# Optimization experiments

Hardware: AMD Instinct MI355X
Metric: run time of the kernel (lower is better)

The kernel has to match this reference:

```python
import jax, jax.numpy as jnp
import numpy as np
from jax import lax

N, P, Z, L = 1000, 50000, 10, 5


def setup_inputs() -> dict:
    key = jax.random.key(0)
    ks = jax.random.split(key, 9)
    data = jax.random.normal(ks[0], (N, P), dtype=jnp.float32)
    mean_z = jax.random.normal(ks[1], (N, Z), dtype=jnp.float32)
    A = jax.random.normal(ks[2], (Z, Z), dtype=jnp.float32) * 0.1
    var_z = A @ A.T + 0.01 * jnp.eye(Z, dtype=jnp.float32)  # PSD
    mean_w = jax.random.normal(ks[3], (L, Z, P), dtype=jnp.float32) * 0.01
    var_w = jax.random.uniform(ks[4], (L, Z), dtype=jnp.float32) + 0.1   # positive
    alpha = jax.nn.softmax(jax.random.normal(ks[5], (L, Z, P), dtype=jnp.float32), axis=-1)
    tau_0 = jax.random.uniform(ks[6], (L, Z), dtype=jnp.float32) + 0.5   # positive prior precision
    pi = jax.nn.softmax(jax.random.normal(ks[7], (Z, P), dtype=jnp.float32), axis=-1)
    tau = jnp.array(1.0, dtype=jnp.float32)
    return dict(data=data, mean_z=mean_z, var_z=var_z, mean_w=mean_w,
                var_w=var_w, alpha=alpha, tau_0=tau_0, pi=pi, tau=tau)


def _log_bf(z, s2, s0):
    s0_inv = 1.0 / s0
    s2ps0inv = s2 + s0_inv
    return 0.5 * (jnp.log(s2) - jnp.log(s2ps0inv) + z ** 2 * (s0_inv / s2ps0inv))


def reference(data, mean_z, var_z, mean_w, var_w, alpha, tau_0, pi, tau):
    n_dim = data.shape[0]
    l_dim, z_dim, p_dim = mean_w.shape

    # FactorModel.moments
    mean_zz = mean_z.T @ mean_z + n_dim * var_z            # [z, z]
    # LoadingModel.moments (only mean_w moment is needed)
    W0 = jnp.sum(mean_w * alpha, axis=0)                    # [z, p]

    def factor_body(kdx, carry):
        W, mw, vw, al = carry
        not_k = jnp.where(jnp.arange(z_dim) != kdx, size=z_dim - 1)[0]  # [z-1]
        E_zpzk = mean_zz[kdx][not_k]                        # [z-1]
        E_zzk = mean_zz[kdx, kdx]                           # scalar
        Wk = W[kdx]                                         # [p]
        Wnk = W[not_k]                                      # [z-1, p]
        RtZk = mean_z[:, kdx] @ data - Wnk.T @ E_zpzk       # [p]

        def effect_body(ldx, ecarry):
            Wk, mw, vw, al = ecarry
            Wkl = Wk - mw[ldx, kdx] * al[ldx, kdx]          # [p] residualized
            E_RtZk = RtZk - E_zzk * Wkl                     # [p]
            u_var = jnp.reciprocal(tau * E_zzk + tau_0[ldx, kdx])  # scalar
            u_mean = tau * u_var * E_RtZk                   # [p]
            Z_s = E_RtZk / E_zzk * jnp.sqrt(E_zzk * tau)    # [p]
            s2_s = 1.0 / (E_zzk * tau)
            log_bf = _log_bf(Z_s, s2_s, tau_0[ldx, kdx])
            alpha_kl = jax.nn.softmax(jnp.log(pi[kdx]) + log_bf)   # [p]
            Wk_new = Wkl + u_mean * alpha_kl
            return (Wk_new,
                    mw.at[ldx, kdx].set(u_mean),
                    vw.at[ldx, kdx].set(u_var),
                    al.at[ldx, kdx].set(alpha_kl))

        Wk, mw, vw, al = lax.fori_loop(0, l_dim, effect_body, (Wk, mw, vw, al))
        return (W.at[kdx].set(Wk), mw, vw, al)

    W, mw, vw, al = lax.fori_loop(0, z_dim, factor_body, (W0, mean_w, var_w, alpha))
    return mw, vw, al
```

## Files before the change

### kernel.cpp

```cpp
#include <hip/hip_runtime.h>
#include <math.h>

#define N_DIM 1000
#define P_DIM 50000
#define Z_DIM 10
#define L_DIM 5
#define NT 256
#define NB 196
#define NSPLIT 4
#define NCHUNK 250
#define NEG_BIG (-3.0e38f)

constexpr size_t ZP      = (size_t)Z_DIM * P_DIM;
constexpr size_t OFF_ZTR = 0;
constexpr size_t OFF_W   = ZP;
constexpr size_t OFF_WK  = 2 * ZP;
constexpr size_t OFF_RTZ = 2 * ZP + P_DIM;
constexpr size_t OFF_LG  = 2 * ZP + 2 * P_DIM;
constexpr size_t OFF_ZZ  = 2 * ZP + 3 * P_DIM;
constexpr size_t OFF_PM0 = OFF_ZZ + 128;
constexpr size_t OFF_PS0 = OFF_PM0 + NB;
constexpr size_t OFF_PM1 = OFF_PS0 + NB;
constexpr size_t OFF_PS1 = OFF_PM1 + NB;

constexpr size_t OUT_MW = 0;
constexpr size_t OUT_VW = (size_t)L_DIM * Z_DIM * P_DIM;
constexpr size_t OUT_AL = OUT_VW + (size_t)L_DIM * Z_DIM;

__device__ inline void online_merge(float& m, float& e, float m2, float e2) {
    float M = fmaxf(m, m2);
    e = e * __expf(m - M) + e2 * __expf(m2 - M);
    m = M;
}

__device__ inline void block_merge(float& m, float& e, float* sm, float* se, float* bro) {
    int lane = threadIdx.x & 63;
    int wid  = threadIdx.x >> 6;
    #pragma unroll
    for (int off = 32; off > 0; off >>= 1) {
        float m2 = __shfl_xor(m, off);
        float e2 = __shfl_xor(e, off);
        online_merge(m, e, m2, e2);
    }
    if (lane == 0) { sm[wid] = m; se[wid] = e; }
    __syncthreads();
    if (threadIdx.x == 0) {
        float M = sm[0], E = se[0];
        #pragma unroll
        for (int w = 1; w < NT / 64; w++) online_merge(M, E, sm[w], se[w]);
        bro[0] = M; bro[1] = E;
    }
    __syncthreads();
    m = bro[0]; e = bro[1];
}

__global__ __launch_bounds__(256) void init_zz(const float* __restrict__ mean_z,
                                               const float* __restrict__ var_z,
                                               float* __restrict__ ws) {
    float* zz = ws + OFF_ZZ;
    int i = blockIdx.x / Z_DIM, j = blockIdx.x % Z_DIM;
    float s = 0.f;
    for (int n = threadIdx.x; n < N_DIM; n += 256)
        s += mean_z[n * Z_DIM + i] * mean_z[n * Z_DIM + j];
    #pragma unroll
    for (int off = 32; off > 0; off >>= 1) s += __shfl_xor(s, off);
    __shared__ float ls[4];
    if ((threadIdx.x & 63) == 0) ls[threadIdx.x >> 6] = s;
    __syncthreads();
    if (threadIdx.x == 0) {
        float t = ls[0] + ls[1] + ls[2] + ls[3];
        zz[blockIdx.x] = t + (float)N_DIM * var_z[blockIdx.x];
    }
}

__global__ __launch_bounds__(NT) void precompute_big(const float* __restrict__ data,
                                                     const float* __restrict__ mean_z,
                                                     const float* __restrict__ mw0,
                                                     const float* __restrict__ al0,
                                                     float* __restrict__ ws) {
    float* ZtR = ws + OFF_ZTR;
    float* W   = ws + OFF_W;
    __shared__ float mzs[NCHUNK * Z_DIM];
    int n0 = blockIdx.y * NCHUNK;
    for (int i = threadIdx.x; i < NCHUNK * Z_DIM; i += NT)
        mzs[i] = mean_z[n0 * Z_DIM + i];
    __syncthreads();
    int p = blockIdx.x * NT + threadIdx.x;
    if (p >= P_DIM) return;

    float acc[Z_DIM];
    #pragma unroll
    for (int z = 0; z < Z_DIM; z++) acc[z] = 0.f;
    for (int r = 0; r < NCHUNK; r++) {
        float d = data[(size_t)(n0 + r) * P_DIM + p];
        #pragma unroll
        for (int z = 0; z < Z_DIM; z++) acc[z] += mzs[r * Z_DIM + z] * d;
    }
    #pragma unroll
    for (int z = 0; z < Z_DIM; z++) atomicAdd(&ZtR[(size_t)z * P_DIM + p], acc[z]);

    if (blockIdx.y == 0) {
        #pragma unroll
        for (int z = 0; z < Z_DIM; z++) {
            float w = 0.f;
            #pragma unroll
            for (int l = 0; l < L_DIM; l++) {
                size_t io = ((size_t)l * Z_DIM + z) * P_DIM + p;
                w += mw0[io] * al0[io];
            }
            W[(size_t)z * P_DIM + p] = w;
        }
    }
}

__global__ __launch_bounds__(NT) void step_kernel(const float* __restrict__ mw0,
                                                  const float* __restrict__ al0,
                                                  const float* __restrict__ pi,
                                                  const float* __restrict__ tau0,
                                                  const float* __restrict__ taup,
                                                  float* __restrict__ ws,
                                                  float* __restrict__ out,
                                                  int k, int l, int pk, int pl,
                                                  int has_prev, int prev_last, int s) {
    float* ZtR = ws + OFF_ZTR;
    float* W   = ws + OFF_W;
    float* Wk  = ws + OFF_WK;
    float* RtZ = ws + OFF_RTZ;
    float* lg  = ws + OFF_LG;
    float* zz  = ws + OFF_ZZ;
    int wbuf = s & 1, rbuf = 1 - wbuf;
    float* pm_r = ws + (rbuf ? OFF_PM1 : OFF_PM0);
    float* ps_r = ws + (rbuf ? OFF_PS1 : OFF_PS0);
    float* pm_w = ws + (wbuf ? OFF_PM1 : OFF_PM0);
    float* ps_w = ws + (wbuf ? OFF_PS1 : OFF_PS0);

    float* out_mw = out + OUT_MW;
    float* out_vw = out + OUT_VW;
    float* out_al = out + OUT_AL;

    __shared__ float sm[NT / 64], se[NT / 64], bro[2];

    int tid = threadIdx.x;
    int p = blockIdx.x * NT + tid;
    bool valid = p < P_DIM;
    float tau = taup[0];

    float wk = 0.f;

    if (has_prev) {
        float m = NEG_BIG, e = 0.f;
        if (tid < NB) { m = pm_r[tid]; e = ps_r[tid]; }
        block_merge(m, e, sm, se, bro);
        float M = m, S = e;
        if (valid) {
            float a = __expf(lg[p] - M) / S;
            size_t po = ((size_t)pl * Z_DIM + pk) * P_DIM + p;
            out_al[po] = a;
            float um = out_mw[po];
            wk = Wk[p] + um * a;
            if (prev_last) W[(size_t)pk * P_DIM + p] = wk;
        }
    }

    float Ezz   = zz[k * Z_DIM + k];
    float t0v   = tau0[l * Z_DIM + k];
    float u_var = 1.f / (tau * Ezz + t0v);
    float s2    = 1.f / (Ezz * tau);
    float s0inv = 1.f / t0v;
    float cq    = 0.5f * (tau / Ezz) * (s0inv / (s2 + s0inv));

    float r = 0.f;
    if (valid) {
        if (l == 0) {
            r = ZtR[(size_t)k * P_DIM + p];
            #pragma unroll
            for (int j = 0; j < Z_DIM; j++) {
                if (j == k) continue;
                float wj = (has_prev && prev_last && j == pk) ? wk
                                                              : W[(size_t)j * P_DIM + p];
                r -= zz[k * Z_DIM + j] * wj;
            }
            RtZ[p] = r;
            wk = W[(size_t)k * P_DIM + p];
        } else {
            r = RtZ[p];
        }
    }

    float m = NEG_BIG, e = 0.f;
    if (valid) {
        size_t io = ((size_t)l * Z_DIM + k) * P_DIM + p;
        float wkl = wk - mw0[io] * al0[io];
        float E   = r - Ezz * wkl;
        float um  = tau * u_var * E;
        float lgt = __logf(pi[(size_t)k * P_DIM + p]) + cq * E * E;
        out_mw[io] = um;
        lg[p] = lgt;
        Wk[p] = wkl;
        m = lgt; e = 1.f;
    }
    block_merge(m, e, sm, se, bro);
    if (tid == 0) { pm_w[blockIdx.x] = m; ps_w[blockIdx.x] = e; }
    if (tid == 0 && blockIdx.x == 0) out_vw[l * Z_DIM + k] = u_var;
}

__global__ __launch_bounds__(NT) void final_kernel(float* __restrict__ ws,
                                                   float* __restrict__ out, int s_last) {
    float* lg = ws + OFF_LG;
    int rbuf = s_last & 1;
    float* pm_r = ws + (rbuf ? OFF_PM1 : OFF_PM0);
    float* ps_r = ws + (rbuf ? OFF_PS1 : OFF_PS0);
    float* out_al = out + OUT_AL;

    __shared__ float sm[NT / 64], se[NT / 64], bro[2];
    int tid = threadIdx.x;
    int p = blockIdx.x * NT + tid;

    float m = NEG_BIG, e = 0.f;
    if (tid < NB) { m = pm_r[tid]; e = ps_r[tid]; }
    block_merge(m, e, sm, se, bro);
    if (p < P_DIM) {
        float a = __expf(lg[p] - m) / e;
        out_al[((size_t)4 * Z_DIM + 9) * P_DIM + p] = a;
    }
}

extern "C" void kernel_launch(void* const* d_in, const int* in_sizes, int n_in,
                              void* d_out, int out_size, void* d_ws, size_t ws_size,
                              hipStream_t stream) {
    (void)in_sizes; (void)n_in; (void)out_size; (void)ws_size;
    const float* data   = (const float*)d_in[0];
    const float* mean_z = (const float*)d_in[1];
    const float* var_z  = (const float*)d_in[2];
    const float* mw0    = (const float*)d_in[3];
    const float* al0    = (const float*)d_in[5];
    const float* tau0   = (const float*)d_in[6];
    const float* pi     = (const float*)d_in[7];
    const float* taup   = (const float*)d_in[8];
    float* out = (float*)d_out;
    float* ws  = (float*)d_ws;

    hipMemsetAsync(ws, 0, ZP * sizeof(float), stream);
    init_zz<<<Z_DIM * Z_DIM, 256, 0, stream>>>(mean_z, var_z, ws);
    precompute_big<<<dim3(NB, NSPLIT), NT, 0, stream>>>(data, mean_z, mw0, al0, ws);

    for (int s = 0; s < Z_DIM * L_DIM; s++) {
        int k = s / L_DIM, l = s % L_DIM;
        int pk = (s > 0) ? (s - 1) / L_DIM : 0;
        int pl = (s > 0) ? (s - 1) % L_DIM : 0;
        int has_prev  = (s > 0) ? 1 : 0;
        int prev_last = (has_prev && pl == L_DIM - 1) ? 1 : 0;
        step_kernel<<<NB, NT, 0, stream>>>(mw0, al0, pi, tau0, taup, ws, out,
                                           k, l, pk, pl, has_prev, prev_last, s);
    }
    final_kernel<<<NB, NT, 0, stream>>>(ws, out, Z_DIM * L_DIM - 1);
}
```

Baseline: 573.6 us.

## Replace per-step kernel launches with single persistent kernel using spin-wait grid reduction

Replaces the 50 step launches and the final kernel with one persistent kernel of 49 blocks of 1024 threads. Each thread keeps its W row and ZtR values in registers across all steps. Blocks publish their softmax partials as packed 64-bit atomics in workspace and spin-wait on them, so no kernel boundary is needed between steps. This removes launch overhead and the global round-trips for W, Wk, RtZ and lg. The cost is a busy-wait that assumes all 49 blocks are co-resident, and a bounded spin (SPIN_MAX) that could silently read incomplete data.

```diff
diff --git a/kernel.cpp b/kernel.cpp
--- a/kernel.cpp
+++ b/kernel.cpp
@@ -5,23 +5,24 @@
 #define P_DIM 50000
 #define Z_DIM 10
 #define L_DIM 5
-#define NT 256
-#define NB 196
+#define NSTEP 50
+
+#define NTP 256
+#define NBP 196
 #define NSPLIT 4
 #define NCHUNK 250
+
+#define NT1 1024
+#define NBLK 49
 #define NEG_BIG (-3.0e38f)
-
-constexpr size_t ZP      = (size_t)Z_DIM * P_DIM;
-constexpr size_t OFF_ZTR = 0;
-constexpr size_t OFF_W   = ZP;
-constexpr size_t OFF_WK  = 2 * ZP;
-constexpr size_t OFF_RTZ = 2 * ZP + P_DIM;
-constexpr size_t OFF_LG  = 2 * ZP + 2 * P_DIM;
-constexpr size_t OFF_ZZ  = 2 * ZP + 3 * P_DIM;
-constexpr size_t OFF_PM0 = OFF_ZZ + 128;
-constexpr size_t OFF_PS0 = OFF_PM0 + NB;
-constexpr size_t OFF_PM1 = OFF_PS0 + NB;
-constexpr size_t OFF_PS1 = OFF_PM1 + NB;
+#define SPIN_MAX 32768
+
+constexpr size_t ZP       = (size_t)Z_DIM * P_DIM;
+constexpr size_t OFF_ZTR  = 0;
+constexpr size_t OFF_PART = ZP;
+constexpr size_t PART_F   = (size_t)NSTEP * 64 * 2;
+constexpr size_t OFF_ZZ   = ZP + PART_F;
+constexpr size_t WS_ZERO_BYTES = (ZP + PART_F) * sizeof(float);
 
 constexpr size_t OUT_MW = 0;
 constexpr size_t OUT_VW = (size_t)L_DIM * Z_DIM * P_DIM;
@@ -31,27 +32,6 @@
     float M = fmaxf(m, m2);
     e = e * __expf(m - M) + e2 * __expf(m2 - M);
     m = M;
-}
-
-__device__ inline void block_merge(float& m, float& e, float* sm, float* se, float* bro) {
-    int lane = threadIdx.x & 63;
-    int wid  = threadIdx.x >> 6;
-    #pragma unroll
-    for (int off = 32; off > 0; off >>= 1) {
-        float m2 = __shfl_xor(m, off);
-        float e2 = __shfl_xor(e, off);
-        online_merge(m, e, m2, e2);
-    }
-    if (lane == 0) { sm[wid] = m; se[wid] = e; }
-    __syncthreads();
-    if (threadIdx.x == 0) {
-        float M = sm[0], E = se[0];
-        #pragma unroll
-        for (int w = 1; w < NT / 64; w++) online_merge(M, E, sm[w], se[w]);
-        bro[0] = M; bro[1] = E;
-    }
-    __syncthreads();
-    m = bro[0]; e = bro[1];
 }
 
 __global__ __launch_bounds__(256) void init_zz(const float* __restrict__ mean_z,
@@ -73,19 +53,16 @@
     }
 }
 
-__global__ __launch_bounds__(NT) void precompute_big(const float* __restrict__ data,
-                                                     const float* __restrict__ mean_z,
-                                                     const float* __restrict__ mw0,
-                                                     const float* __restrict__ al0,
-                                                     float* __restrict__ ws) {
+__global__ __launch_bounds__(NTP) void precompute_big(const float* __restrict__ data,
+                                                      const float* __restrict__ mean_z,
+                                                      float* __restrict__ ws) {
     float* ZtR = ws + OFF_ZTR;
-    float* W   = ws + OFF_W;
     __shared__ float mzs[NCHUNK * Z_DIM];
     int n0 = blockIdx.y * NCHUNK;
-    for (int i = threadIdx.x; i < NCHUNK * Z_DIM; i += NT)
+    for (int i = threadIdx.x; i < NCHUNK * Z_DIM; i += NTP)
         mzs[i] = mean_z[n0 * Z_DIM + i];
     __syncthreads();
-    int p = blockIdx.x * NT + threadIdx.x;
+    int p = blockIdx.x * NTP + threadIdx.x;
     if (p >= P_DIM) return;
 
     float acc[Z_DIM];
@@ -94,134 +71,152 @@
     for (int r = 0; r < NCHUNK; r++) {
         float d = data[(size_t)(n0 + r) * P_DIM + p];
         #pragma unroll
-        for (int z = 0; z < Z_DIM; z++) acc[z] += mzs[r * Z_DIM + z] * d;
+        for (int z = 0; z < Z_DIM; z++) acc[z] = fmaf(mzs[r * Z_DIM + z], d, acc[z]);
     }
     #pragma unroll
     for (int z = 0; z < Z_DIM; z++) atomicAdd(&ZtR[(size_t)z * P_DIM + p], acc[z]);
-
-    if (blockIdx.y == 0) {
-        #pragma unroll
-        for (int z = 0; z < Z_DIM; z++) {
-            float w = 0.f;
-            #pragma unroll
-            for (int l = 0; l < L_DIM; l++) {
-                size_t io = ((size_t)l * Z_DIM + z) * P_DIM + p;
-                w += mw0[io] * al0[io];
-            }
-            W[(size_t)z * P_DIM + p] = w;
-        }
-    }
-}
-
-__global__ __launch_bounds__(NT) void step_kernel(const float* __restrict__ mw0,
+}
+
+__global__ __launch_bounds__(NT1) void steps_coop(const float* __restrict__ mw0,
                                                   const float* __restrict__ al0,
                                                   const float* __restrict__ pi,
                                                   const float* __restrict__ tau0,
                                                   const float* __restrict__ taup,
                                                   float* __restrict__ ws,
-                                                  float* __restrict__ out,
-                                                  int k, int l, int pk, int pl,
-                                                  int has_prev, int prev_last, int s) {
-    float* ZtR = ws + OFF_ZTR;
-    float* W   = ws + OFF_W;
-    float* Wk  = ws + OFF_WK;
-    float* RtZ = ws + OFF_RTZ;
-    float* lg  = ws + OFF_LG;
-    float* zz  = ws + OFF_ZZ;
-    int wbuf = s & 1, rbuf = 1 - wbuf;
-    float* pm_r = ws + (rbuf ? OFF_PM1 : OFF_PM0);
-    float* ps_r = ws + (rbuf ? OFF_PS1 : OFF_PS0);
-    float* pm_w = ws + (wbuf ? OFF_PM1 : OFF_PM0);
-    float* ps_w = ws + (wbuf ? OFF_PS1 : OFF_PS0);
-
+                                                  float* __restrict__ out) {
+    const float* ZtR = ws + OFF_ZTR;
+    const float* zz  = ws + OFF_ZZ;
+    unsigned long long* part = reinterpret_cast<unsigned long long*>(ws + OFF_PART);
     float* out_mw = out + OUT_MW;
     float* out_vw = out + OUT_VW;
     float* out_al = out + OUT_AL;
 
-    __shared__ float sm[NT / 64], se[NT / 64], bro[2];
-
-    int tid = threadIdx.x;
-    int p = blockIdx.x * NT + tid;
-    bool valid = p < P_DIM;
-    float tau = taup[0];
-
-    float wk = 0.f;
-
-    if (has_prev) {
+    __shared__ float sm[NT1 / 64], se[NT1 / 64], bro[2];
+
+    const int tid  = threadIdx.x;
+    const int bid  = blockIdx.x;
+    const int lane = tid & 63;
+    const int wid  = tid >> 6;
+    const int p    = bid * NT1 + tid;
+    const bool valid = p < P_DIM;
+    const float tau = taup[0];
+
+    float W[Z_DIM], Zt[Z_DIM];
+    #pragma unroll
+    for (int z = 0; z < Z_DIM; z++) { W[z] = 0.f; Zt[z] = 0.f; }
+    float mw_c = 0.f, al_c = 0.f, lpi = 0.f;
+    if (valid) {
+        #pragma unroll
+        for (int z = 0; z < Z_DIM; z++) Zt[z] = ZtR[(size_t)z * P_DIM + p];
+        #pragma unroll
+        for (int z = 0; z < Z_DIM; z++) {
+            float w = 0.f;
+            #pragma unroll
+            for (int l = 0; l < L_DIM; l++) {
+                size_t io = ((size_t)l * Z_DIM + z) * P_DIM + p;
+                w = fmaf(mw0[io], al0[io], w);
+            }
+            W[z] = w;
+        }
+        mw_c = mw0[p];
+        al_c = al0[p];
+        lpi  = __logf(pi[p]);
+    }
+
+    float wk = 0.f, r = 0.f;
+    int k = 0, l = 0;
+
+    #pragma unroll 1
+    for (int s = 0; s < NSTEP; s++) {
+        const float Ezz   = zz[k * Z_DIM + k];
+        const float t0v   = tau0[l * Z_DIM + k];
+        const float u_var = 1.f / (tau * Ezz + t0v);
+        const float s2    = 1.f / (Ezz * tau);
+        const float s0inv = 1.f / t0v;
+        const float cq    = 0.5f * (tau / Ezz) * (s0inv / (s2 + s0inv));
+
+        if (l == 0) {
+            float rr = 0.f, wkk = 0.f;
+            #pragma unroll
+            for (int j = 0; j < Z_DIM; j++) {
+                float zkj = zz[k * Z_DIM + j];
+                if (j == k) { rr += Zt[j]; wkk = W[j]; }
+                else        { rr = fmaf(-zkj, W[j], rr); }
+            }
+            r = rr; wk = wkk;
+        }
+
+        const size_t io = ((size_t)l * Z_DIM + k) * P_DIM + p;
+        float wkl = 0.f, um = 0.f, lgt = NEG_BIG;
         float m = NEG_BIG, e = 0.f;
-        if (tid < NB) { m = pm_r[tid]; e = ps_r[tid]; }
-        block_merge(m, e, sm, se, bro);
-        float M = m, S = e;
         if (valid) {
-            float a = __expf(lg[p] - M) / S;
-            size_t po = ((size_t)pl * Z_DIM + pk) * P_DIM + p;
-            out_al[po] = a;
-            float um = out_mw[po];
-            wk = Wk[p] + um * a;
-            if (prev_last) W[(size_t)pk * P_DIM + p] = wk;
-        }
-    }
-
-    float Ezz   = zz[k * Z_DIM + k];
-    float t0v   = tau0[l * Z_DIM + k];
-    float u_var = 1.f / (tau * Ezz + t0v);
-    float s2    = 1.f / (Ezz * tau);
-    float s0inv = 1.f / t0v;
-    float cq    = 0.5f * (tau / Ezz) * (s0inv / (s2 + s0inv));
-
-    float r = 0.f;
-    if (valid) {
-        if (l == 0) {
-            r = ZtR[(size_t)k * P_DIM + p];
-            #pragma unroll
-            for (int j = 0; j < Z_DIM; j++) {
-                if (j == k) continue;
-                float wj = (has_prev && prev_last && j == pk) ? wk
-                                                              : W[(size_t)j * P_DIM + p];
-                r -= zz[k * Z_DIM + j] * wj;
+            wkl = wk - mw_c * al_c;
+            float E = fmaf(-Ezz, wkl, r);
+            um  = tau * u_var * E;
+            lgt = fmaf(cq * E, E, lpi);
+            out_mw[io] = um;
+            m = lgt; e = 1.f;
+        }
+
+        #pragma unroll
+        for (int off = 32; off > 0; off >>= 1)
+            online_merge(m, e, __shfl_xor(m, off), __shfl_xor(e, off));
+        if (lane == 0) { sm[wid] = m; se[wid] = e; }
+        __syncthreads();
+        if (tid == 0) {
+            float M = sm[0], E = se[0];
+            #pragma unroll
+            for (int w = 1; w < NT1 / 64; w++) online_merge(M, E, sm[w], se[w]);
+            unsigned long long v = ((unsigned long long)__float_as_uint(E) << 32)
+                                 | (unsigned long long)__float_as_uint(M);
+            __hip_atomic_store(&part[(size_t)s * 64 + bid], v, __ATOMIC_RELAXED,
+                               __HIP_MEMORY_SCOPE_AGENT);
+        }
+
+        int kn = k, ln = l + 1;
+        if (ln == L_DIM) { ln = 0; kn++; }
+        float mw_n = 0.f, al_n = 0.f, lpi_n = lpi;
+        if (valid && s + 1 < NSTEP) {
+            size_t ion = ((size_t)ln * Z_DIM + kn) * P_DIM + p;
+            mw_n = mw0[ion];
+            al_n = al0[ion];
+            if (ln == 0) lpi_n = __logf(pi[(size_t)kn * P_DIM + p]);
+        }
+
+        float pm = NEG_BIG, pe = 0.f;
+        if (wid == 0) {
+            if (lane < NBLK) {
+                const unsigned long long* ap = &part[(size_t)s * 64 + lane];
+                unsigned long long v = 0;
+                for (int it = 0; it < SPIN_MAX; it++) {
+                    v = __hip_atomic_load(ap, __ATOMIC_RELAXED, __HIP_MEMORY_SCOPE_AGENT);
+                    if ((unsigned)(v >> 32) != 0u) break;
+                }
+                pm = __uint_as_float((unsigned)v);
+                pe = __uint_as_float((unsigned)(v >> 32));
             }
-            RtZ[p] = r;
-            wk = W[(size_t)k * P_DIM + p];
-        } else {
-            r = RtZ[p];
-        }
-    }
-
-    float m = NEG_BIG, e = 0.f;
-    if (valid) {
-        size_t io = ((size_t)l * Z_DIM + k) * P_DIM + p;
-        float wkl = wk - mw0[io] * al0[io];
-        float E   = r - Ezz * wkl;
-        float um  = tau * u_var * E;
-        float lgt = __logf(pi[(size_t)k * P_DIM + p]) + cq * E * E;
-        out_mw[io] = um;
-        lg[p] = lgt;
-        Wk[p] = wkl;
-        m = lgt; e = 1.f;
-    }
-    block_merge(m, e, sm, se, bro);
-    if (tid == 0) { pm_w[blockIdx.x] = m; ps_w[blockIdx.x] = e; }
-    if (tid == 0 && blockIdx.x == 0) out_vw[l * Z_DIM + k] = u_var;
-}
-
-__global__ __launch_bounds__(NT) void final_kernel(float* __restrict__ ws,
-                                                   float* __restrict__ out, int s_last) {
-    float* lg = ws + OFF_LG;
-    int rbuf = s_last & 1;
-    float* pm_r = ws + (rbuf ? OFF_PM1 : OFF_PM0);
-    float* ps_r = ws + (rbuf ? OFF_PS1 : OFF_PS0);
-    float* out_al = out + OUT_AL;
-
-    __shared__ float sm[NT / 64], se[NT / 64], bro[2];
-    int tid = threadIdx.x;
-    int p = blockIdx.x * NT + tid;
-
-    float m = NEG_BIG, e = 0.f;
-    if (tid < NB) { m = pm_r[tid]; e = ps_r[tid]; }
-    block_merge(m, e, sm, se, bro);
-    if (p < P_DIM) {
-        float a = __expf(lg[p] - m) / e;
-        out_al[((size_t)4 * Z_DIM + 9) * P_DIM + p] = a;
+            #pragma unroll
+            for (int off = 32; off > 0; off >>= 1)
+                online_merge(pm, pe, __shfl_xor(pm, off), __shfl_xor(pe, off));
+            if (lane == 0) { bro[0] = pm; bro[1] = pe; }
+        }
+        __syncthreads();
+        const float M    = bro[0];
+        const float Sinv = 1.f / bro[1];
+
+        if (valid) {
+            float a = __expf(lgt - M) * Sinv;
+            out_al[io] = a;
+            wk = fmaf(um, a, wkl);
+        }
+        if (p == 0) out_vw[l * Z_DIM + k] = u_var;
+
+        if (l == L_DIM - 1) {
+            #pragma unroll
+            for (int j = 0; j < Z_DIM; j++) if (j == k) W[j] = wk;
+        }
+        mw_c = mw_n; al_c = al_n; lpi = lpi_n;
+        k = kn; l = ln;
     }
 }
 
@@ -240,18 +235,8 @@
     float* out = (float*)d_out;
     float* ws  = (float*)d_ws;
 
-    hipMemsetAsync(ws, 0, ZP * sizeof(float), stream);
+    hipMemsetAsync(ws, 0, WS_ZERO_BYTES, stream);
     init_zz<<<Z_DIM * Z_DIM, 256, 0, stream>>>(mean_z, var_z, ws);
-    precompute_big<<<dim3(NB, NSPLIT), NT, 0, stream>>>(data, mean_z, mw0, al0, ws);
-
-    for (int s = 0; s < Z_DIM * L_DIM; s++) {
-        int k = s / L_DIM, l = s % L_DIM;
-        int pk = (s > 0) ? (s - 1) / L_DIM : 0;
-        int pl = (s > 0) ? (s - 1) % L_DIM : 0;
-        int has_prev  = (s > 0) ? 1 : 0;
-        int prev_last = (has_prev && pl == L_DIM - 1) ? 1 : 0;
-        step_kernel<<<NB, NT, 0, stream>>>(mw0, al0, pi, tau0, taup, ws, out,
-                                           k, l, pk, pl, has_prev, prev_last, s);
-    }
-    final_kernel<<<NB, NT, 0, stream>>>(ws, out, Z_DIM * L_DIM - 1);
-}
+    precompute_big<<<dim3(NBP, NSPLIT), NTP, 0, stream>>>(data, mean_z, ws);
+    steps_coop<<<NBLK, NT1, 0, stream>>>(mw0, al0, pi, tau0, taup, ws, out);
+}
```

New measurement: 531.7 us. 1.08x faster.
